# Kernel tuning notes

Hardware: AMD Instinct MI355X
Metric: run time of the kernel (lower is better)

## Reference

```python
import jax, jax.numpy as jnp
import numpy as np

D_MODEL = 2048
N_HEADS = 16
N_KV = 4
D_HEAD = 128
D1 = 64
D2 = 64
WSIZE = 1024
EPS = 1e-6
ROPE_BASE = 10000.0


def _rmsnorm(x):
    # RMSNorm over last dim, no affine weight
    return x * jax.lax.rsqrt(jnp.mean(x * x, axis=-1, keepdims=True) + EPS)


def _apply_rope(x, cos, sin):
    # x: (..., D2); cos/sin: (1, T, 1, D2//2)
    h = D2 // 2
    x1, x2 = x[..., :h], x[..., h:]
    return jnp.concatenate([x1 * cos + x2 * sin, -x1 * sin + x2 * cos], axis=-1)


def setup_inputs() -> dict:
    key = jax.random.key(0)
    ks = jax.random.split(key, 6)
    B, T = 2, 2048
    return {
        "hidden_states": jax.random.normal(ks[0], (B, T, D_MODEL), dtype=jnp.float32),
        "W_qkv": jax.random.normal(ks[1], (D_MODEL, (N_HEADS + N_KV) * D_HEAD), dtype=jnp.float32) * 0.02,
        "W_rk": jax.random.normal(ks[2], (D_MODEL, D2), dtype=jnp.float32) * 0.02,
        "b_rk": jax.random.normal(ks[3], (D2,), dtype=jnp.float32) * 0.02,
        "softmax_scaler": jnp.ones((N_HEADS,), dtype=jnp.float32),
        "W_g": jax.random.normal(ks[5], (D_MODEL, D_MODEL), dtype=jnp.float32) * 0.02,
    }


def reference(hidden_states, W_qkv, W_rk, b_rk, softmax_scaler, W_g):
    x = hidden_states
    B, T, _ = x.shape
    # fused qkv projection + per-(head,token) RMSNorm (qk_norm)
    qkv = (x @ W_qkv).reshape(B, T, N_HEADS + N_KV, D_HEAD)
    qkv = _rmsnorm(qkv)
    q, kv = qkv[:, :, :N_HEADS], qkv[:, :, N_HEADS:]
    q_nope, q_rope = q[..., :D1], q[..., D1:]

    # head-tied rope key: shared across all heads
    k_rope = (x @ W_rk + b_rk)[:, :, None, :]  # (B, T, 1, D2)

    # rotary embedding (start_pos = 0)
    inv_freq = 1.0 / (ROPE_BASE ** (jnp.arange(0, D2, 2, dtype=jnp.float32) / D2))
    freqs = jnp.arange(T, dtype=jnp.float32)[:, None] * inv_freq[None, :]  # (T, D2//2)
    cos = jnp.cos(freqs)[None, :, None, :]
    sin = jnp.sin(freqs)[None, :, None, :]
    q_rope = _apply_rope(q_rope, cos, sin)
    k_rope = jnp.broadcast_to(_apply_rope(k_rope, cos, sin), (B, T, N_HEADS, D2))

    q = jnp.concatenate([q_nope, q_rope], axis=-1)  # (B, T, H, D_HEAD)

    # scalable softmax: scale q by per-head scaler * log(min(pos, wsize))
    pos = jnp.arange(1, T + 1, dtype=jnp.float32)
    log_pos = jnp.log(jnp.minimum(pos, float(WSIZE)))[None, :, None, None]
    q = softmax_scaler[None, None, :, None] * log_pos * q

    # tied k/v: first D1 of kv shared between k and v; repeat kv heads (GQA)
    kv_tied, v = kv[..., :D1], kv[..., D1:]
    rep = N_HEADS // N_KV
    kv_tied = jnp.repeat(kv_tied, rep, axis=2)  # (B, T, H, D1)
    v = jnp.repeat(v, rep, axis=2)              # (B, T, H, D2)
    k = jnp.concatenate([kv_tied, k_rope], axis=-1)   # (B, T, H, D_HEAD)
    v_full = jnp.concatenate([kv_tied, v], axis=-1)   # (B, T, H, D_HEAD)

    # sliding-window causal attention: key j valid iff i - WSIZE <= j <= i
    scores = jnp.einsum('bthd,bshd->bhts', q, k) / np.float32(np.sqrt(D_HEAD))
    i = jnp.arange(T)[:, None]
    j = jnp.arange(T)[None, :]
    mask = (j <= i) & (j >= i - WSIZE)
    scores = jnp.where(mask[None, None], scores, jnp.float32(-1e30))
    p = jax.nn.softmax(scores, axis=-1)
    y = jnp.einsum('bhts,bshd->bthd', p, v_full)  # (B, T, H, D_HEAD)

    # elementwise silu gate
    g = (x @ W_g).reshape(B, T, N_HEADS, D_HEAD)
    return y * jax.nn.silu(g)
```

## Files before the change

kernel.cpp:

```cpp
#include <hip/hip_runtime.h>

typedef _Float16 f16;
typedef _Float16 half8 __attribute__((ext_vector_type(8)));
typedef _Float16 half4_t __attribute__((ext_vector_type(4)));
typedef float f32x4 __attribute__((ext_vector_type(4)));

#define T_SEQ 2048
#define B_SZ 2
#define DM 2048
#define NH 16
#define NKV 4
#define DH 128
#define NQKV 2560
#define NALL 4736
#define NALLP 4864
#define COL_RK 2560
#define COL_G 2688
#define M_ROWS 4096
#define WIN 1024

typedef __attribute__((address_space(1))) const unsigned int guint;
typedef __attribute__((address_space(3))) unsigned int luint;
__device__ __forceinline__ void gload16(const void* g, void* l) {
  __builtin_amdgcn_global_load_lds((guint*)g, (luint*)l, 16, 0, 0);
}

__global__ void k_cvt(const float* __restrict__ in, f16* __restrict__ out, int n) {
  int i = (blockIdx.x * 256 + threadIdx.x) * 4;
  if (i >= n) return;
  float4 v = *(const float4*)(in + i);
  half4_t o;
  o[0] = (f16)v.x; o[1] = (f16)v.y; o[2] = (f16)v.z; o[3] = (f16)v.w;
  *(half4_t*)(out + i) = o;
}

__global__ __launch_bounds__(256) void k_cvt_t(const float* __restrict__ W,
                                               f16* __restrict__ Wt, int K, int N) {
  __shared__ float tile[32][33];
  int k0 = blockIdx.x * 32, n0 = blockIdx.y * 32;
  int tx = threadIdx.x & 31, ty = threadIdx.x >> 5;
#pragma unroll
  for (int r = 0; r < 32; r += 8)
    tile[ty + r][tx] = W[(size_t)(k0 + ty + r) * N + n0 + tx];
  __syncthreads();
#pragma unroll
  for (int r = 0; r < 32; r += 8)
    Wt[(size_t)(n0 + ty + r) * K + k0 + tx] = (f16)tile[tx][ty + r];
}

__global__ __launch_bounds__(256) void k_vt(const f16* __restrict__ v, f16* __restrict__ vt) {
  __shared__ f16 tile[32][34];
  int t0 = blockIdx.x * 32, d0 = blockIdx.y * 32, m = blockIdx.z;
  int tx = threadIdx.x & 31, ty = threadIdx.x >> 5;
  const f16* src = v + (size_t)m * T_SEQ * DH;
  f16* dst = vt + (size_t)m * T_SEQ * DH;
#pragma unroll
  for (int r = 0; r < 32; r += 8)
    tile[ty + r][tx] = src[(size_t)(t0 + ty + r) * DH + d0 + tx];
  __syncthreads();
#pragma unroll
  for (int r = 0; r < 32; r += 8)
    dst[(size_t)(d0 + ty + r) * T_SEQ + t0 + tx] = tile[tx][ty + r];
}

#define GEMM_PHASE3(cb, sb, nt)                                                             \
  {                                                                                         \
    char* Ab = lds + (cb) * 16384;                                                          \
    char* Bb = lds + 49152 + (cb) * 8192;                                                   \
    int koff = (nt) * 32;                                                                   \
    half8 af[4], bf[4];                                                                     \
    _Pragma("unroll")                                                                       \
    for (int i = 0; i < 4; ++i)                                                             \
      af[i] = *(const half8*)(Ab + (wm * 64 + i * 16 + fr) * 64 + xsl);                     \
    _Pragma("unroll")                                                                       \
    for (int j = 0; j < 4; ++j)                                                             \
      bf[j] = *(const half8*)(Bb + (wn * 64 + j * 16 + fr) * 64 + xsl);                     \
    gload16(Ag0 + koff, lds + (sb) * 16384 + w * 1024);                                     \
    gload16(Ag1 + koff, lds + (sb) * 16384 + 8192 + w * 1024);                              \
    gload16(Bg + koff, lds + 49152 + (sb) * 8192 + w * 1024);                               \
    __builtin_amdgcn_s_barrier();                                                           \
    __builtin_amdgcn_sched_barrier(0);                                                      \
    asm volatile("s_waitcnt lgkmcnt(0)" ::: "memory");                                      \
    __builtin_amdgcn_sched_barrier(0);                                                      \
    __builtin_amdgcn_s_setprio(1);                                                          \
    _Pragma("unroll")                                                                       \
    for (int i = 0; i < 4; ++i)                                                             \
      _Pragma("unroll")                                                                     \
      for (int j = 0; j < 4; ++j)                                                           \
        acc[i][j] = __builtin_amdgcn_mfma_f32_16x16x32_f16(af[i], bf[j], acc[i][j], 0, 0, 0); \
    __builtin_amdgcn_s_setprio(0);                                                          \
    asm volatile("s_waitcnt vmcnt(3)" ::: "memory");                                        \
    __builtin_amdgcn_s_barrier();                                                           \
    __builtin_amdgcn_sched_barrier(0);                                                      \
  }

__global__ __launch_bounds__(512, 4) void k_gemm8(const f16* __restrict__ A,
                                                  const f16* __restrict__ Bt,
                                                  f16* __restrict__ C) {
  __shared__ __align__(16) char lds[73728];
  const int K = DM;
  unsigned orig = blockIdx.y * 38u + blockIdx.x;
  unsigned swz = (orig & 7u) * 76u + (orig >> 3);
  int m0 = (int)(swz / 38u) * 256;
  int n0 = (int)(swz % 38u) * 128;
  int tid = threadIdx.x, lane = tid & 63, w = tid >> 6;
  int wm = w >> 1, wn = w & 1;
  int fr = lane & 15, fq = lane >> 4;
  int xsl = (fq ^ ((fr >> 1) & 3)) << 4;
  int sr = tid >> 2, ss = tid & 3;
  int scol = (ss ^ ((sr >> 1) & 3)) * 8;
  f32x4 acc[4][4] = {};
  const f16* Ag0 = A + (size_t)(m0 + sr) * K + scol;
  const f16* Ag1 = A + (size_t)(m0 + 128 + sr) * K + scol;
  const f16* Bg  = Bt + (size_t)(n0 + sr) * K + scol;

  gload16(Ag0, lds + w * 1024);
  gload16(Ag1, lds + 8192 + w * 1024);
  gload16(Bg, lds + 49152 + w * 1024);
  gload16(Ag0 + 32, lds + 16384 + w * 1024);
  gload16(Ag1 + 32, lds + 16384 + 8192 + w * 1024);
  gload16(Bg + 32, lds + 49152 + 8192 + w * 1024);
  asm volatile("s_waitcnt vmcnt(3)" ::: "memory");
  __builtin_amdgcn_s_barrier();
  __builtin_amdgcn_sched_barrier(0);

#pragma unroll 1
  for (int t3 = 0; t3 < 21; ++t3) {
    int ktb = t3 * 3;
    int n1_ = ktb + 3 <= 63 ? ktb + 3 : 63;
    int n2_ = ktb + 4 <= 63 ? ktb + 4 : 63;
    GEMM_PHASE3(0, 2, ktb + 2);
    GEMM_PHASE3(1, 0, n1_);
    GEMM_PHASE3(2, 1, n2_);
  }
  GEMM_PHASE3(0, 2, 63);

#pragma unroll
  for (int i = 0; i < 4; ++i) {
    int row = m0 + wm * 64 + i * 16 + fq * 4;
#pragma unroll
    for (int j = 0; j < 4; ++j) {
      int col = n0 + wn * 64 + j * 16 + fr;
      f16* Cp = C + (size_t)row * NALLP + col;
#pragma unroll
      for (int rr = 0; rr < 4; ++rr) Cp[(size_t)rr * NALLP] = (f16)acc[i][j][rr];
    }
  }
}

__global__ __launch_bounds__(256) void k_postproc(
    const f16* __restrict__ CA,
    const float* __restrict__ brk, const float* __restrict__ sscal,
    f16* __restrict__ q16, f16* __restrict__ k16, f16* __restrict__ v16) {
  int row = blockIdx.x;
  int b = row >> 11, t = row & 2047;
  int lane = threadIdx.x & 63, wid = threadIdx.x >> 6;
  int ridx = lane & 31;
  float inv_freq = powf(10000.0f, -(float)(2 * ridx) / 64.0f);
  float fr = (float)t * inv_freq;
  float cs = cosf(fr), sn = sinf(fr);
  float logpos = logf(fminf((float)(t + 1), 1024.0f));
  const float rsqrt_d_log2e = 0.08838834764831845f * 1.4426950408889634f;
  const f16* Crow = CA + (size_t)row * NALLP;
#pragma unroll
  for (int p = 0; p < 5; ++p) {
    int h = p * 4 + wid;
    float v0 = (float)Crow[h * 128 + lane];
    float v1 = (float)Crow[h * 128 + 64 + lane];
    float ss = v0 * v0 + v1 * v1;
#pragma unroll
    for (int m = 1; m < 64; m <<= 1) ss += __shfl_xor(ss, m);
    float rms = rsqrtf(ss * (1.0f / 128.0f) + 1e-6f);
    v0 *= rms; v1 *= rms;
    if (h < NH) {
      float part = __shfl_xor(v1, 32);
      float vr = (lane < 32) ? (v1 * cs + part * sn) : (v1 * cs - part * sn);
      float scale = sscal[h] * logpos * rsqrt_d_log2e;
      size_t qb = ((size_t)(b * NH + h) * T_SEQ + t) * DH;
      q16[qb + lane]      = (f16)(v0 * scale);
      q16[qb + 64 + lane] = (f16)(vr * scale);
    } else {
      int hk = h - NH;
      size_t kb = ((size_t)(b * NKV + hk) * T_SEQ + t) * DH;
      k16[kb + lane]      = (f16)v0;
      v16[kb + lane]      = (f16)v0;
      v16[kb + 64 + lane] = (f16)v1;
    }
  }
  if (wid == 0) {
    float kr = (float)Crow[COL_RK + lane] + brk[lane];
    float part = __shfl_xor(kr, 32);
    float vr = (lane < 32) ? (kr * cs + part * sn) : (kr * cs - part * sn);
    f16 hv = (f16)vr;
#pragma unroll
    for (int hk = 0; hk < NKV; ++hk)
      k16[((size_t)(b * NKV + hk) * T_SEQ + t) * DH + 64 + lane] = hv;
  }
}

__global__ __launch_bounds__(512, 2) void k_attn(
    const f16* __restrict__ q16, const f16* __restrict__ k16, const f16* __restrict__ vt16,
    const f16* __restrict__ gA, float* __restrict__ out) {
  __shared__ __align__(16) char lds[81920];
  int bx = blockIdx.x;
  int qt = (bx & 1) ? (15 - (bx >> 1)) : (bx >> 1);
  int h = blockIdx.y, b = blockIdx.z, hk = h >> 2;
  int tid = threadIdx.x, lane = tid & 63, w = tid >> 6;
  int i0 = qt * 128, iw = i0 + w * 16;
  int fr = lane & 15, fq = lane >> 4;

  char* Psb = lds + 65536 + w * 2048;

  const f16* qbase = q16 + ((size_t)(b * NH + h) * T_SEQ + iw + fr) * DH;
  half8 qf[4];
#pragma unroll
  for (int kb = 0; kb < 4; ++kb) qf[kb] = *(const half8*)&qbase[kb * 32 + fq * 8];

  f32x4 o[8] = {};
  float mrow[4] = {-1e30f, -1e30f, -1e30f, -1e30f};
  float lrow[4] = {0.f, 0.f, 0.f, 0.f};

  const f16* kg = k16 + (size_t)(b * NKV + hk) * T_SEQ * DH;
  const f16* vg = vt16 + (size_t)(b * NKV + hk) * T_SEQ * DH;

  int jtTop = qt * 2 + 1;
  int jt0 = qt >= 8 ? qt * 2 - 16 : 0;

  int kr_ = tid >> 4, kc_ = ((tid & 15) ^ (kr_ & 7)) * 8;
  int vr_ = tid >> 3, vc_ = ((tid & 7) ^ (vr_ & 7)) * 8;

  auto STAGE = [&](int cbuf, int j0) {
    char* Kb = lds + cbuf * 32768;
    char* Vb = lds + cbuf * 32768 + 16384;
#pragma unroll
    for (int i = 0; i < 2; ++i)
      gload16(kg + (size_t)(j0 + i * 32 + kr_) * DH + kc_, Kb + i * 8192 + w * 1024);
#pragma unroll
    for (int i = 0; i < 2; ++i)
      gload16(vg + (size_t)(i * 64 + vr_) * T_SEQ + j0 + vc_, Vb + i * 8192 + w * 1024);
  };

  STAGE(0, jt0 * 64);
  asm volatile("s_waitcnt vmcnt(0)" ::: "memory");
  __syncthreads();
  int cur = 0;

  for (int jt = jt0; jt <= jtTop; ++jt) {
    if (jt < jtTop) STAGE(cur ^ 1, (jt + 1) * 64);
    char* Ksb = lds + cur * 32768;
    char* Vsb = lds + cur * 32768 + 16384;

    bool active = (jt == jtTop) ? (w >= 4)
                : ((qt >= 8 && jt == jt0) ? (w < 4) : true);
    if (active) {
      f32x4 s[4] = {};
      __builtin_amdgcn_s_setprio(1);
#pragma unroll
      for (int nf = 0; nf < 4; ++nf) {
        int row = nf * 16 + fr;
        int sw = fr & 7;
#pragma unroll
        for (int kb = 0; kb < 4; ++kb) {
          half8 bfv = *(const half8*)(Ksb + row * 256 + ((((kb << 2) | fq) ^ sw) << 4));
          s[nf] = __builtin_amdgcn_mfma_f32_16x16x32_f16(qf[kb], bfv, s[nf], 0, 0, 0);
        }
      }
      __builtin_amdgcn_s_setprio(0);
      int il = (w << 4) + (fq << 2);
      if (jt >= (qt << 1)) {
        int dc = (jt << 6) - i0;
#pragma unroll
        for (int nf = 0; nf < 4; ++nf) {
          int jo = nf * 16 + fr + dc;
#pragma unroll
          for (int r = 0; r < 4; ++r)
            if (jo > il + r) s[nf][r] = -3e38f;
        }
      } else if (qt >= 8 && jt - jt0 < 2) {
        int dl = (jt - jt0) << 6;
#pragma unroll
        for (int nf = 0; nf < 4; ++nf) {
          int jo = nf * 16 + fr + dl;
#pragma unroll
          for (int r = 0; r < 4; ++r)
            if (jo < il + r) s[nf][r] = -3e38f;
        }
      }
      float tm[4];
#pragma unroll
      for (int r = 0; r < 4; ++r)
        tm[r] = fmaxf(fmaxf(s[0][r], s[1][r]), fmaxf(s[2][r], s[3][r]));
#pragma unroll
      for (int r = 0; r < 4; ++r) {
        tm[r] = fmaxf(tm[r], __shfl_xor(tm[r], 1));
        tm[r] = fmaxf(tm[r], __shfl_xor(tm[r], 2));
        tm[r] = fmaxf(tm[r], __shfl_xor(tm[r], 4));
        tm[r] = fmaxf(tm[r], __shfl_xor(tm[r], 8));
      }
      bool need = false;
#pragma unroll
      for (int r = 0; r < 4; ++r) need = need || (tm[r] > mrow[r] + 8.0f);
      if (__any(need)) {
#pragma unroll
        for (int r = 0; r < 4; ++r) {
          float mn = fmaxf(mrow[r], tm[r]);
          float sc = exp2f(mrow[r] - mn);
          mrow[r] = mn;
          lrow[r] *= sc;
#pragma unroll
          for (int of = 0; of < 8; ++of) o[of][r] *= sc;
        }
      }
      float ls[4] = {0.f, 0.f, 0.f, 0.f};
#pragma unroll
      for (int nf = 0; nf < 4; ++nf)
#pragma unroll
        for (int r = 0; r < 4; ++r) {
          float pv = exp2f(s[nf][r] - mrow[r]);
          s[nf][r] = pv;
          ls[r] += pv;
        }
#pragma unroll
      for (int r = 0; r < 4; ++r) {
        float t2 = ls[r];
        t2 += __shfl_xor(t2, 1); t2 += __shfl_xor(t2, 2);
        t2 += __shfl_xor(t2, 4); t2 += __shfl_xor(t2, 8);
        lrow[r] += t2;
      }
#pragma unroll
      for (int nf = 0; nf < 4; ++nf) {
        int sbase = (nf << 1) + (fr >> 3);
        int boff = (fr & 7) << 1;
#pragma unroll
        for (int r = 0; r < 4; ++r) {
          int q = (fq << 2) + r;
          *(f16*)(Psb + q * 128 + ((sbase ^ (q & 7)) << 4) + boff) = (f16)s[nf][r];
        }
      }
      asm volatile("s_waitcnt lgkmcnt(0)" ::: "memory");
      __builtin_amdgcn_sched_barrier(0);
      half8 pf0 = *(const half8*)(Psb + fr * 128 + (((fq) ^ (fr & 7)) << 4));
      half8 pf1 = *(const half8*)(Psb + fr * 128 + (((4 | fq) ^ (fr & 7)) << 4));
      __builtin_amdgcn_s_setprio(1);
#pragma unroll
      for (int of = 0; of < 8; ++of) {
        int vrow0 = of * 16 + fr;
        int sw = fr & 7;
        half8 v0 = *(const half8*)(Vsb + vrow0 * 128 + ((fq ^ sw) << 4));
        half8 v1 = *(const half8*)(Vsb + vrow0 * 128 + (((4 | fq) ^ sw) << 4));
        o[of] = __builtin_amdgcn_mfma_f32_16x16x32_f16(pf0, v0, o[of], 0, 0, 0);
        o[of] = __builtin_amdgcn_mfma_f32_16x16x32_f16(pf1, v1, o[of], 0, 0, 0);
      }
      __builtin_amdgcn_s_setprio(0);
    }
    asm volatile("s_waitcnt vmcnt(0)" ::: "memory");
    __syncthreads();
    cur ^= 1;
  }
  const f16* gb = gA + ((size_t)(b * T_SEQ) + iw) * NALLP + COL_G + h * DH;
  float* ob = out + ((size_t)(b * T_SEQ) + iw) * DM + h * DH;
#pragma unroll
  for (int r = 0; r < 4; ++r) {
    float inv = 1.0f / lrow[r];
    int ir = fq * 4 + r;
#pragma unroll
    for (int of = 0; of < 8; ++of) {
      int d = of * 16 + fr;
      float gv = (float)gb[(size_t)ir * NALLP + d];
      float sig = gv / (1.0f + expf(-gv));
      ob[(size_t)ir * DM + d] = o[of][r] * inv * sig;
    }
  }
}

extern "C" void kernel_launch(void* const* d_in, const int* in_sizes, int n_in,
                              void* d_out, int out_size, void* d_ws, size_t ws_size,
                              hipStream_t stream) {
  const float* x     = (const float*)d_in[0];
  const float* Wqkv  = (const float*)d_in[1];
  const float* Wrk   = (const float*)d_in[2];
  const float* brk   = (const float*)d_in[3];
  const float* sscal = (const float*)d_in[4];
  const float* Wg    = (const float*)d_in[5];
  float* out = (float*)d_out;
  char* ws = (char*)d_ws;
  size_t off = 0;
  auto alloc = [&](size_t bytes) -> void* {
    void* p = ws + off;
    off += (bytes + 255) & ~(size_t)255;
    return p;
  };
  f16* x16     = (f16*)alloc((size_t)M_ROWS * DM * 2);
  f16* BtAll   = (f16*)alloc((size_t)NALLP * DM * 2);
  f16* CAll    = (f16*)alloc((size_t)M_ROWS * NALLP * 2);
  f16* q16     = (f16*)alloc((size_t)B_SZ * NH * T_SEQ * DH * 2);
  f16* k16     = (f16*)alloc((size_t)B_SZ * NKV * T_SEQ * DH * 2);
  f16* v16     = (f16*)alloc((size_t)B_SZ * NKV * T_SEQ * DH * 2);
  f16* vt16    = (f16*)alloc((size_t)B_SZ * NKV * T_SEQ * DH * 2);

  k_cvt<<<(M_ROWS * DM / 4 + 255) / 256, 256, 0, stream>>>(x, x16, M_ROWS * DM);
  k_cvt_t<<<dim3(DM / 32, NQKV / 32), 256, 0, stream>>>(Wqkv, BtAll, DM, NQKV);
  k_cvt_t<<<dim3(DM / 32, 64 / 32), 256, 0, stream>>>(Wrk, BtAll + (size_t)COL_RK * DM, DM, 64);
  k_cvt_t<<<dim3(DM / 32, DM / 32), 256, 0, stream>>>(Wg, BtAll + (size_t)COL_G * DM, DM, DM);

  k_gemm8<<<dim3(NALLP / 128, M_ROWS / 256), 512, 0, stream>>>(x16, BtAll, CAll);

  k_postproc<<<M_ROWS, 256, 0, stream>>>(CAll, brk, sscal, q16, k16, v16);
  k_vt<<<dim3(T_SEQ / 32, DH / 32, B_SZ * NKV), 256, 0, stream>>>(v16, vt16);

  k_attn<<<dim3(T_SEQ / 128, NH, B_SZ), 512, 0, stream>>>(q16, k16, vt16, CAll, out);
}
```

Measured before the change: 338.7 us.

## Shrink attention query tile to 64 rows, drop double buffering, use cheaper rope math

The attention kernel now uses 64-query-row tiles with 4 waves (256 threads), twice as many blocks, and a single LDS buffer loaded synchronously each key tile instead of double-buffered prefetch. This halves LDS per block and removes idle-wave iterations on diagonal and window-edge tiles, but K/V reuse per load drops and load latency is no longer hidden. The postproc kernel also replaces powf/logf with exp2f/__log2f forms.

Result: no change. 338.7 us (+0.0%).

```diff
diff --git a/kernel.cpp b/kernel.cpp
--- a/kernel.cpp
+++ b/kernel.cpp
@@ -156,10 +156,10 @@
   int b = row >> 11, t = row & 2047;
   int lane = threadIdx.x & 63, wid = threadIdx.x >> 6;
   int ridx = lane & 31;
-  float inv_freq = powf(10000.0f, -(float)(2 * ridx) / 64.0f);
+  float inv_freq = exp2f(-(float)ridx * 0.41524101186092074f);
   float fr = (float)t * inv_freq;
   float cs = cosf(fr), sn = sinf(fr);
-  float logpos = logf(fminf((float)(t + 1), 1024.0f));
+  float logpos = 0.6931471805599453f * __log2f(fminf((float)(t + 1), 1024.0f));
   const float rsqrt_d_log2e = 0.08838834764831845f * 1.4426950408889634f;
   const f16* Crow = CA + (size_t)row * NALLP;
 #pragma unroll
@@ -198,18 +198,18 @@
   }
 }
 
-__global__ __launch_bounds__(512, 2) void k_attn(
+__global__ __launch_bounds__(256, 2) void k_attn(
     const f16* __restrict__ q16, const f16* __restrict__ k16, const f16* __restrict__ vt16,
     const f16* __restrict__ gA, float* __restrict__ out) {
-  __shared__ __align__(16) char lds[81920];
+  __shared__ __align__(16) char lds[40960];
   int bx = blockIdx.x;
-  int qt = (bx & 1) ? (15 - (bx >> 1)) : (bx >> 1);
+  int qt = (bx & 1) ? (31 - (bx >> 1)) : (bx >> 1);
   int h = blockIdx.y, b = blockIdx.z, hk = h >> 2;
   int tid = threadIdx.x, lane = tid & 63, w = tid >> 6;
-  int i0 = qt * 128, iw = i0 + w * 16;
+  int i0 = qt * 64, iw = i0 + w * 16;
   int fr = lane & 15, fq = lane >> 4;
 
-  char* Psb = lds + 65536 + w * 2048;
+  char* Psb = lds + 32768 + w * 2048;
 
   const f16* qbase = q16 + ((size_t)(b * NH + h) * T_SEQ + iw + fr) * DH;
   half8 qf[4];
@@ -223,139 +223,123 @@
   const f16* kg = k16 + (size_t)(b * NKV + hk) * T_SEQ * DH;
   const f16* vg = vt16 + (size_t)(b * NKV + hk) * T_SEQ * DH;
 
-  int jtTop = qt * 2 + 1;
-  int jt0 = qt >= 8 ? qt * 2 - 16 : 0;
-
-  int kr_ = tid >> 4, kc_ = ((tid & 15) ^ (kr_ & 7)) * 8;
-  int vr_ = tid >> 3, vc_ = ((tid & 7) ^ (vr_ & 7)) * 8;
-
-  auto STAGE = [&](int cbuf, int j0) {
-    char* Kb = lds + cbuf * 32768;
-    char* Vb = lds + cbuf * 32768 + 16384;
-#pragma unroll
-    for (int i = 0; i < 2; ++i)
-      gload16(kg + (size_t)(j0 + i * 32 + kr_) * DH + kc_, Kb + i * 8192 + w * 1024);
-#pragma unroll
-    for (int i = 0; i < 2; ++i)
-      gload16(vg + (size_t)(i * 64 + vr_) * T_SEQ + j0 + vc_, Vb + i * 8192 + w * 1024);
-  };
-
-  STAGE(0, jt0 * 64);
-  asm volatile("s_waitcnt vmcnt(0)" ::: "memory");
-  __syncthreads();
-  int cur = 0;
-
-  for (int jt = jt0; jt <= jtTop; ++jt) {
-    if (jt < jtTop) STAGE(cur ^ 1, (jt + 1) * 64);
-    char* Ksb = lds + cur * 32768;
-    char* Vsb = lds + cur * 32768 + 16384;
-
-    bool active = (jt == jtTop) ? (w >= 4)
-                : ((qt >= 8 && jt == jt0) ? (w < 4) : true);
-    if (active) {
-      f32x4 s[4] = {};
-      __builtin_amdgcn_s_setprio(1);
-#pragma unroll
-      for (int nf = 0; nf < 4; ++nf) {
-        int row = nf * 16 + fr;
-        int sw = fr & 7;
-#pragma unroll
-        for (int kb = 0; kb < 4; ++kb) {
-          half8 bfv = *(const half8*)(Ksb + row * 256 + ((((kb << 2) | fq) ^ sw) << 4));
-          s[nf] = __builtin_amdgcn_mfma_f32_16x16x32_f16(qf[kb], bfv, s[nf], 0, 0, 0);
-        }
-      }
-      __builtin_amdgcn_s_setprio(0);
-      int il = (w << 4) + (fq << 2);
-      if (jt >= (qt << 1)) {
-        int dc = (jt << 6) - i0;
-#pragma unroll
-        for (int nf = 0; nf < 4; ++nf) {
-          int jo = nf * 16 + fr + dc;
-#pragma unroll
-          for (int r = 0; r < 4; ++r)
-            if (jo > il + r) s[nf][r] = -3e38f;
-        }
-      } else if (qt >= 8 && jt - jt0 < 2) {
-        int dl = (jt - jt0) << 6;
-#pragma unroll
-        for (int nf = 0; nf < 4; ++nf) {
-          int jo = nf * 16 + fr + dl;
-#pragma unroll
-          for (int r = 0; r < 4; ++r)
-            if (jo < il + r) s[nf][r] = -3e38f;
-        }
-      }
-      float tm[4];
-#pragma unroll
-      for (int r = 0; r < 4; ++r)
-        tm[r] = fmaxf(fmaxf(s[0][r], s[1][r]), fmaxf(s[2][r], s[3][r]));
-#pragma unroll
-      for (int r = 0; r < 4; ++r) {
-        tm[r] = fmaxf(tm[r], __shfl_xor(tm[r], 1));
-        tm[r] = fmaxf(tm[r], __shfl_xor(tm[r], 2));
-        tm[r] = fmaxf(tm[r], __shfl_xor(tm[r], 4));
-        tm[r] = fmaxf(tm[r], __shfl_xor(tm[r], 8));
-      }
-      bool need = false;
-#pragma unroll
-      for (int r = 0; r < 4; ++r) need = need || (tm[r] > mrow[r] + 8.0f);
-      if (__any(need)) {
-#pragma unroll
-        for (int r = 0; r < 4; ++r) {
-          float mn = fmaxf(mrow[r], tm[r]);
-          float sc = exp2f(mrow[r] - mn);
-          mrow[r] = mn;
-          lrow[r] *= sc;
-#pragma unroll
-          for (int of = 0; of < 8; ++of) o[of][r] *= sc;
-        }
-      }
-      float ls[4] = {0.f, 0.f, 0.f, 0.f};
-#pragma unroll
-      for (int nf = 0; nf < 4; ++nf)
-#pragma unroll
-        for (int r = 0; r < 4; ++r) {
-          float pv = exp2f(s[nf][r] - mrow[r]);
-          s[nf][r] = pv;
-          ls[r] += pv;
-        }
-#pragma unroll
-      for (int r = 0; r < 4; ++r) {
-        float t2 = ls[r];
-        t2 += __shfl_xor(t2, 1); t2 += __shfl_xor(t2, 2);
-        t2 += __shfl_xor(t2, 4); t2 += __shfl_xor(t2, 8);
-        lrow[r] += t2;
-      }
-#pragma unroll
-      for (int nf = 0; nf < 4; ++nf) {
-        int sbase = (nf << 1) + (fr >> 3);
-        int boff = (fr & 7) << 1;
-#pragma unroll
-        for (int r = 0; r < 4; ++r) {
-          int q = (fq << 2) + r;
-          *(f16*)(Psb + q * 128 + ((sbase ^ (q & 7)) << 4) + boff) = (f16)s[nf][r];
-        }
-      }
-      asm volatile("s_waitcnt lgkmcnt(0)" ::: "memory");
-      __builtin_amdgcn_sched_barrier(0);
-      half8 pf0 = *(const half8*)(Psb + fr * 128 + (((fq) ^ (fr & 7)) << 4));
-      half8 pf1 = *(const half8*)(Psb + fr * 128 + (((4 | fq) ^ (fr & 7)) << 4));
-      __builtin_amdgcn_s_setprio(1);
-#pragma unroll
-      for (int of = 0; of < 8; ++of) {
-        int vrow0 = of * 16 + fr;
-        int sw = fr & 7;
-        half8 v0 = *(const half8*)(Vsb + vrow0 * 128 + ((fq ^ sw) << 4));
-        half8 v1 = *(const half8*)(Vsb + vrow0 * 128 + (((4 | fq) ^ sw) << 4));
-        o[of] = __builtin_amdgcn_mfma_f32_16x16x32_f16(pf0, v0, o[of], 0, 0, 0);
-        o[of] = __builtin_amdgcn_mfma_f32_16x16x32_f16(pf1, v1, o[of], 0, 0, 0);
-      }
-      __builtin_amdgcn_s_setprio(0);
+  int jt0 = qt >= 16 ? qt - 16 : 0;
+
+  for (int jt = jt0; jt <= qt; ++jt) {
+    int j0 = jt * 64;
+#pragma unroll
+    for (int i = 0; i < 4; ++i) {
+      int r = i * 16 + (tid >> 4);
+      int c = ((tid & 15) ^ (r & 7)) * 8;
+      gload16(kg + (size_t)(j0 + r) * DH + c, lds + i * 4096 + w * 1024);
+    }
+#pragma unroll
+    for (int i = 0; i < 4; ++i) {
+      int r = i * 32 + (tid >> 3);
+      int c = ((tid & 7) ^ (r & 7)) * 8;
+      gload16(vg + (size_t)r * T_SEQ + j0 + c, lds + 16384 + i * 4096 + w * 1024);
     }
     asm volatile("s_waitcnt vmcnt(0)" ::: "memory");
     __syncthreads();
-    cur ^= 1;
+
+    f32x4 s[4] = {};
+    __builtin_amdgcn_s_setprio(1);
+#pragma unroll
+    for (int nf = 0; nf < 4; ++nf) {
+      int row = nf * 16 + fr;
+      int sw = fr & 7;
+#pragma unroll
+      for (int kb = 0; kb < 4; ++kb) {
+        half8 bfv = *(const half8*)(lds + row * 256 + ((((kb << 2) | fq) ^ sw) << 4));
+        s[nf] = __builtin_amdgcn_mfma_f32_16x16x32_f16(qf[kb], bfv, s[nf], 0, 0, 0);
+      }
+    }
+    __builtin_amdgcn_s_setprio(0);
+    int il = (w << 4) + (fq << 2);
+    if (jt == qt) {
+#pragma unroll
+      for (int nf = 0; nf < 4; ++nf) {
+        int jo = nf * 16 + fr;
+#pragma unroll
+        for (int r = 0; r < 4; ++r)
+          if (jo > il + r) s[nf][r] = -3e38f;
+      }
+    } else if (qt >= 16 && jt == jt0) {
+#pragma unroll
+      for (int nf = 0; nf < 4; ++nf) {
+        int jo = nf * 16 + fr;
+#pragma unroll
+        for (int r = 0; r < 4; ++r)
+          if (jo < il + r) s[nf][r] = -3e38f;
+      }
+    }
+    float tm[4];
+#pragma unroll
+    for (int r = 0; r < 4; ++r)
+      tm[r] = fmaxf(fmaxf(s[0][r], s[1][r]), fmaxf(s[2][r], s[3][r]));
+#pragma unroll
+    for (int r = 0; r < 4; ++r) {
+      tm[r] = fmaxf(tm[r], __shfl_xor(tm[r], 1));
+      tm[r] = fmaxf(tm[r], __shfl_xor(tm[r], 2));
+      tm[r] = fmaxf(tm[r], __shfl_xor(tm[r], 4));
+      tm[r] = fmaxf(tm[r], __shfl_xor(tm[r], 8));
+    }
+    bool need = false;
+#pragma unroll
+    for (int r = 0; r < 4; ++r) need = need || (tm[r] > mrow[r] + 8.0f);
+    if (__any(need)) {
+#pragma unroll
+      for (int r = 0; r < 4; ++r) {
+        float mn = fmaxf(mrow[r], tm[r]);
+        float sc = exp2f(mrow[r] - mn);
+        mrow[r] = mn;
+        lrow[r] *= sc;
+#pragma unroll
+        for (int of = 0; of < 8; ++of) o[of][r] *= sc;
+      }
+    }
+    float ls[4] = {0.f, 0.f, 0.f, 0.f};
+#pragma unroll
+    for (int nf = 0; nf < 4; ++nf)
+#pragma unroll
+      for (int r = 0; r < 4; ++r) {
+        float pv = exp2f(s[nf][r] - mrow[r]);
+        s[nf][r] = pv;
+        ls[r] += pv;
+      }
+#pragma unroll
+    for (int r = 0; r < 4; ++r) {
+      float t2 = ls[r];
+      t2 += __shfl_xor(t2, 1); t2 += __shfl_xor(t2, 2);
+      t2 += __shfl_xor(t2, 4); t2 += __shfl_xor(t2, 8);
+      lrow[r] += t2;
+    }
+#pragma unroll
+    for (int nf = 0; nf < 4; ++nf) {
+      int sbase = (nf << 1) + (fr >> 3);
+      int boff = (fr & 7) << 1;
+#pragma unroll
+      for (int r = 0; r < 4; ++r) {
+        int q = (fq << 2) + r;
+        *(f16*)(Psb + q * 128 + ((sbase ^ (q & 7)) << 4) + boff) = (f16)s[nf][r];
+      }
+    }
+    asm volatile("s_waitcnt lgkmcnt(0)" ::: "memory");
+    __builtin_amdgcn_sched_barrier(0);
+    half8 pf0 = *(const half8*)(Psb + fr * 128 + (((fq) ^ (fr & 7)) << 4));
+    half8 pf1 = *(const half8*)(Psb + fr * 128 + (((4 | fq) ^ (fr & 7)) << 4));
+    __builtin_amdgcn_s_setprio(1);
+#pragma unroll
+    for (int of = 0; of < 8; ++of) {
+      int vrow0 = of * 16 + fr;
+      int sw = fr & 7;
+      half8 v0 = *(const half8*)(lds + 16384 + vrow0 * 128 + ((fq ^ sw) << 4));
+      half8 v1 = *(const half8*)(lds + 16384 + vrow0 * 128 + (((4 | fq) ^ sw) << 4));
+      o[of] = __builtin_amdgcn_mfma_f32_16x16x32_f16(pf0, v0, o[of], 0, 0, 0);
+      o[of] = __builtin_amdgcn_mfma_f32_16x16x32_f16(pf1, v1, o[of], 0, 0, 0);
+    }
+    __builtin_amdgcn_s_setprio(0);
+    __syncthreads();
   }
   const f16* gb = gA + ((size_t)(b * T_SEQ) + iw) * NALLP + COL_G + h * DH;
   float* ob = out + ((size_t)(b * T_SEQ) + iw) * DM + h * DH;
@@ -408,5 +392,5 @@
   k_postproc<<<M_ROWS, 256, 0, stream>>>(CAll, brk, sscal, q16, k16, v16);
   k_vt<<<dim3(T_SEQ / 32, DH / 32, B_SZ * NKV), 256, 0, stream>>>(v16, vt16);
 
-  k_attn<<<dim3(T_SEQ / 128, NH, B_SZ), 512, 0, stream>>>(q16, k16, vt16, CAll, out);
-}
+  k_attn<<<dim3(T_SEQ / 64, NH, B_SZ), 256, 0, stream>>>(q16, k16, vt16, CAll, out);
+}
```
